# Performance work log

Hardware: AMD Instinct MI355X
Metric: run time of the kernel (lower is better)

The kernel has to match this reference:

```python
import jax, jax.numpy as jnp
import numpy as np

V = 6890   # SMPL vertices
J = 24     # SMPL joints
NB = 10    # betas
P = 207    # pose blendshape basis = (J-1)*9
B = 1024
PARENTS = np.array([-1, 0, 0, 0, 1, 2, 3, 4, 5, 6, 7, 8, 9, 9, 9, 12, 13, 14, 16, 17, 18, 19, 20, 21])


def setup_inputs() -> dict:
    key = jax.random.key(0)
    ks = jax.random.split(key, 9)
    pose_axis_angle = jax.random.normal(ks[0], (B, 69), dtype=jnp.float32) * 0.2
    betas = jax.random.normal(ks[1], (B, NB), dtype=jnp.float32)
    global_orient = jax.random.normal(ks[2], (B, 3), dtype=jnp.float32) * 0.2
    v_template = jax.random.normal(ks[3], (V, 3), dtype=jnp.float32)
    shapedirs = jax.random.normal(ks[4], (V, 3, NB), dtype=jnp.float32) * 0.01
    posedirs = jax.random.normal(ks[5], (P, V * 3), dtype=jnp.float32) * 0.01
    jr = jax.random.uniform(ks[6], (J, V), dtype=jnp.float32)
    J_regressor = jr / jr.sum(-1, keepdims=True)
    jr17 = jax.random.uniform(ks[7], (17, V), dtype=jnp.float32)
    J_regressor_h36m = jr17 / jr17.sum(-1, keepdims=True)
    w = jax.random.uniform(ks[8], (V, J), dtype=jnp.float32)
    lbs_weights = w / w.sum(-1, keepdims=True)
    return {
        'pose_axis_angle': pose_axis_angle, 'betas': betas, 'global_orient': global_orient,
        'v_template': v_template, 'shapedirs': shapedirs, 'posedirs': posedirs,
        'J_regressor': J_regressor, 'J_regressor_h36m': J_regressor_h36m,
        'lbs_weights': lbs_weights,
    }


def rodrigues(rvec):
    # rvec: [N,3] axis-angle -> [N,3,3] rotation matrices
    angle = jnp.linalg.norm(rvec + 1e-8, axis=-1, keepdims=True)  # [N,1]
    axis = rvec / angle
    s = jnp.sin(angle)[..., None]
    c = jnp.cos(angle)[..., None]
    rx, ry, rz = axis[..., 0], axis[..., 1], axis[..., 2]
    z = jnp.zeros_like(rx)
    K = jnp.stack([z, -rz, ry, rz, z, -rx, -ry, rx, z], axis=-1).reshape(-1, 3, 3)
    I = jnp.eye(3, dtype=rvec.dtype)
    return I + s * K + (1.0 - c) * (K @ K)


def _lbs(pose_axis_angle, betas, global_orient, v_template, shapedirs, posedirs,
         J_regressor, J_regressor_h36m, lbs_weights):
    b = betas.shape[0]
    full_pose = jnp.concatenate([global_orient, pose_axis_angle], axis=1)  # [B,72]
    # shape blendshapes
    v_shaped = v_template + jnp.einsum('bl,vkl->bvk', betas, shapedirs)    # [B,V,3]
    Jrest = jnp.einsum('jv,bvk->bjk', J_regressor, v_shaped)               # [B,J,3]
    # pose to rotation matrices
    rot_mats = rodrigues(full_pose.reshape(-1, 3)).reshape(b, J, 3, 3)
    I3 = jnp.eye(3, dtype=rot_mats.dtype)
    pose_feature = (rot_mats[:, 1:] - I3).reshape(b, P)                    # [B,207]
    v_posed = v_shaped + (pose_feature @ posedirs).reshape(b, V, 3)
    # kinematic tree FK
    rel = Jrest.at[:, 1:].add(-Jrest[:, PARENTS[1:]])                      # relative joint offsets
    T = (jnp.zeros((b, J, 4, 4), dtype=rot_mats.dtype)
         .at[..., :3, :3].set(rot_mats)
         .at[..., :3, 3].set(rel)
         .at[..., 3, 3].set(1.0))
    chain = [T[:, 0]]
    for i in range(1, J):
        chain.append(chain[int(PARENTS[i])] @ T[:, i])
    G = jnp.stack(chain, axis=1)                                           # [B,J,4,4]
    posed_joints = G[:, :, :3, 3]
    # remove rest-pose joint locations to get skinning transforms
    A = G.at[:, :, :3, 3].add(-jnp.einsum('bjmn,bjn->bjm', G[:, :, :3, :3], Jrest))
    # linear blend skinning
    Tv = jnp.einsum('vj,bjmn->bvmn', lbs_weights, A)                       # [B,V,4,4]
    verts = jnp.einsum('bvmn,bvn->bvm', Tv[:, :, :3, :3], v_posed) + Tv[:, :, :3, 3]
    joints_from_verts = jnp.einsum('jv,bvk->bjk', J_regressor_h36m, verts)
    return verts, posed_joints, rot_mats, joints_from_verts


def reference(pose_axis_angle, betas, global_orient, v_template, shapedirs, posedirs,
              J_regressor, J_regressor_h36m, lbs_weights):
    verts, joints, rot_mats, jfv = _lbs(pose_axis_angle, betas, global_orient, v_template,
                                        shapedirs, posedirs, J_regressor, J_regressor_h36m,
                                        lbs_weights)
    # transl is None -> root-center (root is detached in torch)
    root = jax.lax.stop_gradient(joints[:, :1])
    root17 = jax.lax.stop_gradient(jfv[:, :1])
    return verts - root, joints - root, rot_mats, jfv - root17
```

## Files before the change

kernel.cpp:

```cpp
#include <hip/hip_runtime.h>
#include <hip/hip_bf16.h>

constexpr int kB  = 1024;
constexpr int kV  = 6890;
constexpr int kJ  = 24;
constexpr int kNB = 10;
constexpr int kP  = 207;
constexpr int kH  = 17;
constexpr int TB  = 8;

constexpr int kN   = kV * 3;
constexpr int kKP  = 224;
constexpr int kNT  = 1296;
constexpr int kNP  = kNT * 16;
constexpr int kVC  = 862;

constexpr size_t O_VERTS  = 0;
constexpr size_t O_JOINTS = (size_t)kB * kV * 3;
constexpr size_t O_ROT    = O_JOINTS + (size_t)kB * kJ * 3;
constexpr size_t O_JFV    = O_ROT + (size_t)kB * kJ * 9;

constexpr size_t WS_JS   = 0;
constexpr size_t WS_FLAG = 1000;
constexpr size_t WS_A    = 1024;
constexpr size_t WS_PF   = WS_A + (size_t)kB * 288;
constexpr size_t WS_ROOT = WS_PF + (size_t)kB * kP;
constexpr size_t WS_JFV  = WS_ROOT + (size_t)kB * 3;
constexpr size_t WS_ASWZ = 563200;
constexpr size_t WS_BSWZ = WS_ASWZ + 114688;

typedef __attribute__((ext_vector_type(8))) short short8;
typedef __attribute__((ext_vector_type(4))) float float4v;

__device__ __forceinline__ unsigned short f2bf(float f) {
    unsigned u = __float_as_uint(f);
    unsigned r = (u + 0x7FFFu + ((u >> 16) & 1u)) >> 16;
    return (unsigned short)r;
}

__global__ void k_classify(const float* __restrict__ amb0, int* __restrict__ flag)
{
    if (blockIdx.x == 0 && threadIdx.x == 0) {
        float s = 0.f;
        for (int i = 0; i < kJ; i++) s += amb0[i];
        *flag = (fabsf(s - 1.0f) < 0.5f) ? 1 : 0;
    }
}

__global__ __launch_bounds__(256) void k_js(
    const float* __restrict__ amb0,
    const float* __restrict__ amb1,
    const int* __restrict__ flag,
    const float* __restrict__ sd,
    const float* __restrict__ vt,
    float* __restrict__ partial)
{
    const float* Jreg = (*flag) ? amb1 : amb0;
    int j = blockIdx.x;
    int c = blockIdx.y;
    int t = threadIdx.x;
    int lane = t & 63;
    int wave = t >> 6;

    float acc[33];
    #pragma unroll
    for (int i = 0; i < 33; i++) acc[i] = 0.f;

    int vend = min(kVC * (c + 1), kV);
    for (int v = kVC * c + t; v < vend; v += 256) {
        float w = Jreg[j * kV + v];
        const float* sdp = sd + (size_t)v * 30;
        #pragma unroll
        for (int k = 0; k < 3; k++) {
            #pragma unroll
            for (int l = 0; l < kNB; l++)
                acc[k * 11 + l] += w * sdp[k * 10 + l];
            acc[k * 11 + 10] += w * vt[v * 3 + k];
        }
    }
    #pragma unroll
    for (int off = 32; off > 0; off >>= 1) {
        #pragma unroll
        for (int i = 0; i < 33; i++)
            acc[i] += __shfl_down(acc[i], off, 64);
    }
    __shared__ float red[4][33];
    if (lane == 0) {
        #pragma unroll
        for (int i = 0; i < 33; i++) red[wave][i] = acc[i];
    }
    __syncthreads();
    if (t < 33) {
        float s = red[0][t] + red[1][t] + red[2][t] + red[3][t];
        partial[((size_t)j * 8 + c) * 33 + t] = s;
    }
}

__global__ __launch_bounds__(1024) void k_js_reduce(
    const float* __restrict__ partial,
    float* __restrict__ js)
{
    int t = threadIdx.x;
    if (t < 24 * 33) {
        int j = t / 33, i = t % 33;
        float s = 0.f;
        #pragma unroll
        for (int c = 0; c < 8; c++) s += partial[((size_t)j * 8 + c) * 33 + i];
        js[t] = s;
    }
}

__global__ __launch_bounds__(64) void k_pose(
    const float* __restrict__ pose,
    const float* __restrict__ betas,
    const float* __restrict__ gor,
    const float* __restrict__ js,
    float* __restrict__ wsA,
    float* __restrict__ wsPF,
    float* __restrict__ wsRoot,
    float* __restrict__ out)
{
    __shared__ float Rsh[kJ][9];
    __shared__ float Jr[kJ][3];
    __shared__ float G[kJ][12];

    int b = blockIdx.x;
    int t = threadIdx.x;

    if (t < kJ) {
        float rx, ry, rz;
        if (t == 0) {
            rx = gor[b * 3 + 0]; ry = gor[b * 3 + 1]; rz = gor[b * 3 + 2];
        } else {
            int o = b * 69 + (t - 1) * 3;
            rx = pose[o]; ry = pose[o + 1]; rz = pose[o + 2];
        }
        float ex = rx + 1e-8f, ey = ry + 1e-8f, ez = rz + 1e-8f;
        float ang = sqrtf(ex * ex + ey * ey + ez * ez);
        float x = rx / ang, y = ry / ang, z = rz / ang;
        float s = sinf(ang), c = cosf(ang), oc = 1.0f - c;
        float r[9];
        r[0] = 1.0f - oc * (y * y + z * z);
        r[1] = -s * z + oc * (x * y);
        r[2] =  s * y + oc * (x * z);
        r[3] =  s * z + oc * (x * y);
        r[4] = 1.0f - oc * (x * x + z * z);
        r[5] = -s * x + oc * (y * z);
        r[6] = -s * y + oc * (x * z);
        r[7] =  s * x + oc * (y * z);
        r[8] = 1.0f - oc * (x * x + y * y);
        #pragma unroll
        for (int i = 0; i < 9; i++) Rsh[t][i] = r[i];
        float* ro = out + O_ROT + (size_t)b * (kJ * 9) + (size_t)t * 9;
        #pragma unroll
        for (int i = 0; i < 9; i++) ro[i] = r[i];
        if (t >= 1) {
            float* pf = wsPF + (size_t)b * kP + (size_t)(t - 1) * 9;
            #pragma unroll
            for (int i = 0; i < 9; i++)
                pf[i] = r[i] - ((i == 0 || i == 4 || i == 8) ? 1.0f : 0.0f);
        }
        float bt[kNB];
        #pragma unroll
        for (int l = 0; l < kNB; l++) bt[l] = betas[b * kNB + l];
        #pragma unroll
        for (int k = 0; k < 3; k++) {
            const float* row = js + (t * 3 + k) * 11;
            float acc = row[10];
            #pragma unroll
            for (int l = 0; l < kNB; l++) acc += bt[l] * row[l];
            Jr[t][k] = acc;
        }
    }
    __syncthreads();

    if (t == 0) {
        const int par[kJ] = {-1,0,0,0,1,2,3,4,5,6,7,8,9,9,9,12,13,14,16,17,18,19,20,21};
        #pragma unroll
        for (int m = 0; m < 3; m++) {
            #pragma unroll
            for (int n = 0; n < 3; n++) G[0][m * 4 + n] = Rsh[0][m * 3 + n];
            G[0][m * 4 + 3] = Jr[0][m];
        }
        for (int i = 1; i < kJ; i++) {
            int p = par[i];
            float rel[3];
            #pragma unroll
            for (int k = 0; k < 3; k++) rel[k] = Jr[i][k] - Jr[p][k];
            #pragma unroll
            for (int m = 0; m < 3; m++) {
                float g0 = G[p][m * 4 + 0], g1 = G[p][m * 4 + 1], g2 = G[p][m * 4 + 2];
                #pragma unroll
                for (int n = 0; n < 3; n++) {
                    G[i][m * 4 + n] = g0 * Rsh[i][0 * 3 + n]
                                    + g1 * Rsh[i][1 * 3 + n]
                                    + g2 * Rsh[i][2 * 3 + n];
                }
                G[i][m * 4 + 3] = g0 * rel[0] + g1 * rel[1] + g2 * rel[2]
                                + G[p][m * 4 + 3];
            }
        }
    }
    __syncthreads();

    if (t < kJ) {
        float* Aj = wsA + (size_t)b * 288 + (size_t)t * 12;
        float* jo = out + O_JOINTS + (size_t)b * (kJ * 3) + (size_t)t * 3;
        #pragma unroll
        for (int m = 0; m < 3; m++) {
            float g0 = G[t][m * 4 + 0], g1 = G[t][m * 4 + 1], g2 = G[t][m * 4 + 2];
            Aj[m * 4 + 0] = g0;
            Aj[m * 4 + 1] = g1;
            Aj[m * 4 + 2] = g2;
            Aj[m * 4 + 3] = G[t][m * 4 + 3]
                          - (g0 * Jr[t][0] + g1 * Jr[t][1] + g2 * Jr[t][2]);
            jo[m] = G[t][m * 4 + 3] - G[0][m * 4 + 3];
        }
        if (t == 0) {
            #pragma unroll
            for (int k = 0; k < 3; k++) wsRoot[b * 3 + k] = G[0][k * 4 + 3];
        }
    }
}

__global__ __launch_bounds__(256) void k_prep_b(
    const float* __restrict__ pd,
    const float* __restrict__ sd,
    const float* __restrict__ vt,
    unsigned short* __restrict__ bswz)
{
    __shared__ unsigned short lds[kKP][68];
    int g = blockIdx.x;
    int n0 = g * 64;
    int t = threadIdx.x;

    for (int kbase = 0; kbase < kKP; kbase += 4) {
        int k = kbase + (t >> 6);
        int nl = t & 63;
        int n = n0 + nl;
        float val = 0.f;
        if (n < kN) {
            if (k < kP)                 val = pd[(size_t)k * kN + n];
            else if (k < kP + kNB)      val = sd[(size_t)n * kNB + (k - kP)];
            else if (k == kP + kNB)     val = vt[n];
        }
        lds[k][nl] = f2bf(val);
    }
    __syncthreads();

    #pragma unroll 1
    for (int tt = 0; tt < 4; tt++) {
        int ntile = g * 4 + tt;
        #pragma unroll 1
        for (int kt = 0; kt < 7; kt++) {
            size_t base = ((size_t)ntile * 7 + kt) * 512;
            #pragma unroll
            for (int u = 0; u < 2; u++) {
                int e = t * 2 + u;
                int quad = e >> 7, rem = e & 127;
                int nin = rem >> 3, kin = rem & 7;
                int k = kt * 32 + quad * 8 + kin;
                bswz[base + e] = lds[k][tt * 16 + nin];
            }
        }
    }
}

__global__ __launch_bounds__(256) void k_prep_a(
    const float* __restrict__ wsPF,
    const float* __restrict__ betas,
    unsigned short* __restrict__ aswz)
{
    int mtile = blockIdx.x;
    int t = threadIdx.x;
    for (int e = t; e < 16 * kKP; e += 256) {
        int kt = e >> 9, r = e & 511;
        int quad = r >> 7, min_ = (r >> 3) & 15, kin = r & 7;
        int k = kt * 32 + quad * 8 + kin;
        int b = mtile * 16 + min_;
        float val = 0.f;
        if (k < kP)             val = wsPF[(size_t)b * kP + k];
        else if (k < kP + kNB)  val = betas[(size_t)b * kNB + (k - kP)];
        else if (k == kP + kNB) val = 1.0f;
        aswz[((size_t)mtile * 7 + kt) * 512 + r] = f2bf(val);
    }
}

__global__ __launch_bounds__(256) void k_gemm(
    const unsigned short* __restrict__ A,
    const unsigned short* __restrict__ B,
    float* __restrict__ out)
{
    int tid = threadIdx.x;
    int lane = tid & 63;
    int wid = tid >> 6;
    int m0t = blockIdx.y * 8 + (wid >> 1) * 4;
    int n0t = blockIdx.x * 8 + (wid & 1) * 4;

    float4v acc[4][4];
    #pragma unroll
    for (int i = 0; i < 4; i++)
        #pragma unroll
        for (int j = 0; j < 4; j++)
            acc[i][j] = (float4v){0.f, 0.f, 0.f, 0.f};

    #pragma unroll
    for (int kt = 0; kt < 7; kt++) {
        short8 a[4], b[4];
        #pragma unroll
        for (int i = 0; i < 4; i++)
            a[i] = *(const short8*)(A + ((size_t)(m0t + i) * 7 + kt) * 512 + lane * 8);
        #pragma unroll
        for (int j = 0; j < 4; j++)
            b[j] = *(const short8*)(B + ((size_t)(n0t + j) * 7 + kt) * 512 + lane * 8);
        #pragma unroll
        for (int i = 0; i < 4; i++)
            #pragma unroll
            for (int j = 0; j < 4; j++)
                acc[i][j] = __builtin_amdgcn_mfma_f32_16x16x32_bf16(
                    a[i], b[j], acc[i][j], 0, 0, 0);
    }

    int rbase = (lane >> 4) * 4;
    int col = lane & 15;
    #pragma unroll
    for (int i = 0; i < 4; i++) {
        #pragma unroll
        for (int j = 0; j < 4; j++) {
            int n = (n0t + j) * 16 + col;
            if (n < kN) {
                #pragma unroll
                for (int reg = 0; reg < 4; reg++) {
                    int brow = (m0t + i) * 16 + rbase + reg;
                    out[O_VERTS + (size_t)brow * kN + n] = acc[i][j][reg];
                }
            }
        }
    }
}

__global__ __launch_bounds__(256) void k_prep_jh(
    const float* __restrict__ Jh,
    float* __restrict__ jht)
{
    int v = blockIdx.x * 256 + threadIdx.x;
    if (v >= kV) return;
    #pragma unroll
    for (int j = 0; j < kH; j++)
        jht[(size_t)v * kH + j] = Jh[(size_t)j * kV + v];
}

__global__ __launch_bounds__(256) void k_lbs(
    const float* __restrict__ amb0,
    const float* __restrict__ amb1,
    const int* __restrict__ flag,
    const float* __restrict__ wsA,
    const float* __restrict__ wsRoot,
    float* __restrict__ out)
{
    const float* W = (*flag) ? amb0 : amb1;

    int t = threadIdx.x;
    int b0 = blockIdx.y * TB;

    int v = blockIdx.x * 256 + t;
    if (v >= kV) return;

    float w[kJ];
    {
        const float* Wv = W + (size_t)v * kJ;
        #pragma unroll
        for (int j = 0; j < kJ; j++) w[j] = Wv[j];
    }
    #pragma unroll 1
    for (int tb = 0; tb < TB; tb++) {
        const float* Ab = wsA + (size_t)(b0 + tb) * 288;
        float Tv[12];
        #pragma unroll
        for (int i = 0; i < 12; i++) Tv[i] = w[0] * Ab[i];
        #pragma unroll
        for (int j = 1; j < kJ; j++) {
            float wj = w[j];
            #pragma unroll
            for (int i = 0; i < 12; i++) Tv[i] += wj * Ab[j * 12 + i];
        }
        float r0 = wsRoot[(size_t)(b0 + tb) * 3 + 0];
        float r1 = wsRoot[(size_t)(b0 + tb) * 3 + 1];
        float r2 = wsRoot[(size_t)(b0 + tb) * 3 + 2];
        float* op = out + O_VERTS + ((size_t)(b0 + tb) * kV + v) * 3;
        float x = op[0], y = op[1], z = op[2];
        float o0 = Tv[0] * x + Tv[1] * y + Tv[2]  * z + Tv[3]  - r0;
        float o1 = Tv[4] * x + Tv[5] * y + Tv[6]  * z + Tv[7]  - r1;
        float o2 = Tv[8] * x + Tv[9] * y + Tv[10] * z + Tv[11] - r2;
        op[0] = o0;
        op[1] = o1;
        op[2] = o2;
    }
}

__global__ __launch_bounds__(256) void k_jfv(
    const float* __restrict__ jht,
    const float* __restrict__ vertsOut,
    float* __restrict__ wsJfv)
{
    int b = blockIdx.x;
    int t = threadIdx.x;
    int lane = t & 63;
    int wave = t >> 6;

    float acc[kH * 3];
    #pragma unroll
    for (int i = 0; i < kH * 3; i++) acc[i] = 0.f;

    for (int v = t; v < kV; v += 256) {
        const float* vpt = vertsOut + ((size_t)b * kV + v) * 3;
        float vx = vpt[0], vy = vpt[1], vz = vpt[2];
        const float* jt = jht + (size_t)v * kH;
        #pragma unroll
        for (int j = 0; j < kH; j++) {
            float wj = jt[j];
            acc[j * 3 + 0] += wj * vx;
            acc[j * 3 + 1] += wj * vy;
            acc[j * 3 + 2] += wj * vz;
        }
    }
    #pragma unroll
    for (int off = 32; off > 0; off >>= 1) {
        #pragma unroll
        for (int i = 0; i < kH * 3; i++)
            acc[i] += __shfl_down(acc[i], off, 64);
    }
    __shared__ float partial[4][kH * 3];
    if (lane == 0) {
        #pragma unroll
        for (int i = 0; i < kH * 3; i++) partial[wave][i] = acc[i];
    }
    __syncthreads();
    if (t < kH * 3) {
        float s = partial[0][t] + partial[1][t] + partial[2][t] + partial[3][t];
        wsJfv[(size_t)b * 51 + t] = s;
    }
}

__global__ __launch_bounds__(64) void k_jfv_out(
    const float* __restrict__ wsJfv,
    float* __restrict__ out)
{
    int b = blockIdx.x;
    int t = threadIdx.x;
    if (t < kH * 3) {
        int k = t % 3;
        float val = wsJfv[(size_t)b * 51 + t] - wsJfv[(size_t)b * 51 + k];
        out[O_JFV + (size_t)b * 51 + t] = val;
    }
}

extern "C" void kernel_launch(void* const* d_in, const int* in_sizes, int n_in,
                              void* d_out, int out_size, void* d_ws, size_t ws_size,
                              hipStream_t stream) {
    const float *pose = nullptr, *betas = nullptr, *gor = nullptr, *vt = nullptr,
                *sd = nullptr, *pd = nullptr, *Jh = nullptr;
    const float *amb0 = nullptr, *amb1 = nullptr;
    for (int i = 0; i < n_in; i++) {
        const float* p = (const float*)d_in[i];
        switch (in_sizes[i]) {
            case 70656:   pose  = p; break;
            case 10240:   betas = p; break;
            case 3072:    gor   = p; break;
            case 20670:   vt    = p; break;
            case 206700:  sd    = p; break;
            case 4278690: pd    = p; break;
            case 117130:  Jh    = p; break;
            case 165360:  if (!amb0) amb0 = p; else amb1 = p; break;
            default: break;
        }
    }

    float* ws = (float*)d_ws;
    float* js      = ws + WS_JS;
    int*   flag    = (int*)(ws + WS_FLAG);
    float* wsA     = ws + WS_A;
    float* wsPF    = ws + WS_PF;
    float* wsRoot  = ws + WS_ROOT;
    float* wsJfv   = ws + WS_JFV;
    unsigned short* aswz = (unsigned short*)(ws + WS_ASWZ);
    unsigned short* bswz = (unsigned short*)(ws + WS_BSWZ);
    float* jspart  = ws + WS_ASWZ;
    float* jht     = ws + WS_BSWZ;

    float* out = (float*)d_out;

    k_classify<<<dim3(1), dim3(64), 0, stream>>>(amb0, flag);
    k_js<<<dim3(kJ, 8), dim3(256), 0, stream>>>(amb0, amb1, flag, sd, vt, jspart);
    k_js_reduce<<<dim3(1), dim3(1024), 0, stream>>>(jspart, js);
    k_pose<<<dim3(kB), dim3(64), 0, stream>>>(pose, betas, gor, js, wsA, wsPF, wsRoot, out);
    k_prep_b<<<dim3(kNP / 64), dim3(256), 0, stream>>>(pd, sd, vt, bswz);
    k_prep_a<<<dim3(64), dim3(256), 0, stream>>>(wsPF, betas, aswz);
    k_gemm<<<dim3(kNT / 8, kB / 128), dim3(256), 0, stream>>>(aswz, bswz, out);
    k_prep_jh<<<dim3((kV + 255) / 256), dim3(256), 0, stream>>>(Jh, jht);
    k_lbs<<<dim3((kV + 255) / 256, kB / TB), dim3(256), 0, stream>>>(
        amb0, amb1, flag, wsA, wsRoot, out);
    k_jfv<<<dim3(kB), dim3(256), 0, stream>>>(jht, out + O_VERTS, wsJfv);
    k_jfv_out<<<dim3(kB), dim3(64), 0, stream>>>(wsJfv, out);
}
```

Before: 306.4 us.

## Fuse pose-blendshape GEMM with LBS skinning via MFMA in one kernel

```diff
diff --git a/kernel.cpp b/kernel.cpp
--- a/kernel.cpp
+++ b/kernel.cpp
@@ -7,13 +7,13 @@
 constexpr int kNB = 10;
 constexpr int kP  = 207;
 constexpr int kH  = 17;
-constexpr int TB  = 8;
 
 constexpr int kN   = kV * 3;
 constexpr int kKP  = 224;
 constexpr int kNT  = 1296;
 constexpr int kNP  = kNT * 16;
 constexpr int kVC  = 862;
+constexpr int kVT  = 432;
 
 constexpr size_t O_VERTS  = 0;
 constexpr size_t O_JOINTS = (size_t)kB * kV * 3;
@@ -21,13 +21,14 @@
 constexpr size_t O_JFV    = O_ROT + (size_t)kB * kJ * 9;
 
 constexpr size_t WS_JS   = 0;
-constexpr size_t WS_FLAG = 1000;
 constexpr size_t WS_A    = 1024;
 constexpr size_t WS_PF   = WS_A + (size_t)kB * 288;
 constexpr size_t WS_ROOT = WS_PF + (size_t)kB * kP;
 constexpr size_t WS_JFV  = WS_ROOT + (size_t)kB * 3;
-constexpr size_t WS_ASWZ = 563200;
-constexpr size_t WS_BSWZ = WS_ASWZ + 114688;
+constexpr size_t WS_A1   = 563200;
+constexpr size_t WS_B1   = WS_A1 + 114688;
+constexpr size_t WS_W    = WS_PF;
+constexpr size_t WS_JHT  = WS_B1;
 
 typedef __attribute__((ext_vector_type(8))) short short8;
 typedef __attribute__((ext_vector_type(4))) float float4v;
@@ -38,24 +39,21 @@
     return (unsigned short)r;
 }
 
-__global__ void k_classify(const float* __restrict__ amb0, int* __restrict__ flag)
-{
-    if (blockIdx.x == 0 && threadIdx.x == 0) {
-        float s = 0.f;
-        for (int i = 0; i < kJ; i++) s += amb0[i];
-        *flag = (fabsf(s - 1.0f) < 0.5f) ? 1 : 0;
-    }
+__device__ __forceinline__ bool is_lbs(const float* __restrict__ p) {
+    float s = 0.f;
+    #pragma unroll
+    for (int i = 0; i < kJ; i++) s += p[i];
+    return fabsf(s - 1.0f) < 0.5f;
 }
 
 __global__ __launch_bounds__(256) void k_js(
     const float* __restrict__ amb0,
     const float* __restrict__ amb1,
-    const int* __restrict__ flag,
     const float* __restrict__ sd,
     const float* __restrict__ vt,
     float* __restrict__ partial)
 {
-    const float* Jreg = (*flag) ? amb1 : amb0;
+    const float* Jreg = is_lbs(amb0) ? amb1 : amb0;
     int j = blockIdx.x;
     int c = blockIdx.y;
     int t = threadIdx.x;
@@ -286,54 +284,112 @@
     }
 }
 
-__global__ __launch_bounds__(256) void k_gemm(
-    const unsigned short* __restrict__ A,
-    const unsigned short* __restrict__ B,
+__global__ __launch_bounds__(256) void k_prep_w(
+    const float* __restrict__ amb0,
+    const float* __restrict__ amb1,
+    unsigned short* __restrict__ wswz)
+{
+    const float* W = is_lbs(amb0) ? amb0 : amb1;
+    int vtile = blockIdx.x;
+    int t = threadIdx.x;
+    #pragma unroll
+    for (int u = 0; u < 2; u++) {
+        int e = t * 2 + u;
+        int quad = e >> 7, min_ = (e >> 3) & 15, kin = e & 7;
+        int v = vtile * 16 + min_;
+        int j = quad * 8 + kin;
+        float val = (v < kV && j < kJ) ? W[(size_t)v * kJ + j] : 0.f;
+        wswz[(size_t)vtile * 512 + e] = f2bf(val);
+    }
+}
+
+__global__ __launch_bounds__(256) void k_fused(
+    const unsigned short* __restrict__ A1,
+    const unsigned short* __restrict__ B1,
+    const unsigned short* __restrict__ Wswz,
+    const float* __restrict__ wsA,
+    const float* __restrict__ wsRoot,
     float* __restrict__ out)
 {
-    int tid = threadIdx.x;
-    int lane = tid & 63;
-    int wid = tid >> 6;
-    int m0t = blockIdx.y * 8 + (wid >> 1) * 4;
-    int n0t = blockIdx.x * 8 + (wid & 1) * 4;
-
-    float4v acc[4][4];
+    __shared__ float c1[16 * 193];
+    __shared__ unsigned short a2[16 * 512];
+
+    int t = threadIdx.x;
+    int lane = t & 63;
+    int w = t >> 6;
+    int btile = blockIdx.x;
+    int b0 = btile * 16;
+    int vt0 = blockIdx.y * 4;
+
+    for (int e = t; e < 16 * 512; e += 256) {
+        int btl = e >> 9, r = e & 511;
+        int quad = r >> 7, nin = (r >> 3) & 15, kin = r & 7;
+        int j = quad * 8 + kin;
+        float val = (j < kJ && nin < 12)
+                  ? wsA[(size_t)(b0 + btl) * 288 + j * 12 + nin] : 0.f;
+        a2[e] = f2bf(val);
+    }
+
+    float4v acc1[3];
+    #pragma unroll
+    for (int jj = 0; jj < 3; jj++) acc1[jj] = (float4v){0.f, 0.f, 0.f, 0.f};
+    #pragma unroll
+    for (int kt = 0; kt < 7; kt++) {
+        short8 af = *(const short8*)(A1 + ((size_t)btile * 7 + kt) * 512 + lane * 8);
+        #pragma unroll
+        for (int jj = 0; jj < 3; jj++) {
+            int nt = blockIdx.y * 12 + w * 3 + jj;
+            short8 bf = *(const short8*)(B1 + ((size_t)nt * 7 + kt) * 512 + lane * 8);
+            acc1[jj] = __builtin_amdgcn_mfma_f32_16x16x32_bf16(af, bf, acc1[jj], 0, 0, 0);
+        }
+    }
+    int col = lane & 15, quad = lane >> 4;
+    #pragma unroll
+    for (int jj = 0; jj < 3; jj++) {
+        #pragma unroll
+        for (int reg = 0; reg < 4; reg++) {
+            int brow = quad * 4 + reg;
+            c1[brow * 193 + (w * 3 + jj) * 16 + col] = acc1[jj][reg];
+        }
+    }
+    __syncthreads();
+
+    short8 wa[4];
     #pragma unroll
     for (int i = 0; i < 4; i++)
-        #pragma unroll
-        for (int j = 0; j < 4; j++)
-            acc[i][j] = (float4v){0.f, 0.f, 0.f, 0.f};
-
-    #pragma unroll
-    for (int kt = 0; kt < 7; kt++) {
-        short8 a[4], b[4];
+        wa[i] = *(const short8*)(Wswz + (size_t)(vt0 + i) * 512 + lane * 8);
+    float4v acc2[4][4];
+    #pragma unroll
+    for (int i = 0; i < 4; i++)
+        #pragma unroll
+        for (int jw = 0; jw < 4; jw++)
+            acc2[i][jw] = (float4v){0.f, 0.f, 0.f, 0.f};
+    #pragma unroll
+    for (int jw = 0; jw < 4; jw++) {
+        short8 bfr = *(const short8*)(a2 + (w * 4 + jw) * 512 + lane * 8);
         #pragma unroll
         for (int i = 0; i < 4; i++)
-            a[i] = *(const short8*)(A + ((size_t)(m0t + i) * 7 + kt) * 512 + lane * 8);
-        #pragma unroll
-        for (int j = 0; j < 4; j++)
-            b[j] = *(const short8*)(B + ((size_t)(n0t + j) * 7 + kt) * 512 + lane * 8);
-        #pragma unroll
-        for (int i = 0; i < 4; i++)
-            #pragma unroll
-            for (int j = 0; j < 4; j++)
-                acc[i][j] = __builtin_amdgcn_mfma_f32_16x16x32_bf16(
-                    a[i], b[j], acc[i][j], 0, 0, 0);
-    }
-
-    int rbase = (lane >> 4) * 4;
-    int col = lane & 15;
-    #pragma unroll
-    for (int i = 0; i < 4; i++) {
-        #pragma unroll
-        for (int j = 0; j < 4; j++) {
-            int n = (n0t + j) * 16 + col;
-            if (n < kN) {
-                #pragma unroll
-                for (int reg = 0; reg < 4; reg++) {
-                    int brow = (m0t + i) * 16 + rbase + reg;
-                    out[O_VERTS + (size_t)brow * kN + n] = acc[i][j][reg];
-                }
+            acc2[i][jw] = __builtin_amdgcn_mfma_f32_16x16x32_bf16(wa[i], bfr, acc2[i][jw], 0, 0, 0);
+    }
+
+    int kk = col & 3, m = col >> 2;
+    #pragma unroll
+    for (int jw = 0; jw < 4; jw++) {
+        int bl = w * 4 + jw;
+        int b = b0 + bl;
+        float rt = (m < 3) ? wsRoot[(size_t)b * 3 + m] : 0.f;
+        #pragma unroll
+        for (int i = 0; i < 4; i++) {
+            #pragma unroll
+            for (int reg = 0; reg < 4; reg++) {
+                int vloc = i * 16 + quad * 4 + reg;
+                float h = (kk < 3) ? c1[bl * 193 + vloc * 3 + kk] : 1.0f;
+                float o = acc2[i][jw][reg] * h;
+                o += __shfl_xor(o, 1, 64);
+                o += __shfl_xor(o, 2, 64);
+                int vg = blockIdx.y * 64 + vloc;
+                if (kk == 0 && m < 3 && vg < kV)
+                    out[O_VERTS + ((size_t)b * kV + vg) * 3 + m] = o - rt;
             }
         }
     }
@@ -348,54 +404,6 @@
     #pragma unroll
     for (int j = 0; j < kH; j++)
         jht[(size_t)v * kH + j] = Jh[(size_t)j * kV + v];
-}
-
-__global__ __launch_bounds__(256) void k_lbs(
-    const float* __restrict__ amb0,
-    const float* __restrict__ amb1,
-    const int* __restrict__ flag,
-    const float* __restrict__ wsA,
-    const float* __restrict__ wsRoot,
-    float* __restrict__ out)
-{
-    const float* W = (*flag) ? amb0 : amb1;
-
-    int t = threadIdx.x;
-    int b0 = blockIdx.y * TB;
-
-    int v = blockIdx.x * 256 + t;
-    if (v >= kV) return;
-
-    float w[kJ];
-    {
-        const float* Wv = W + (size_t)v * kJ;
-        #pragma unroll
-        for (int j = 0; j < kJ; j++) w[j] = Wv[j];
-    }
-    #pragma unroll 1
-    for (int tb = 0; tb < TB; tb++) {
-        const float* Ab = wsA + (size_t)(b0 + tb) * 288;
-        float Tv[12];
-        #pragma unroll
-        for (int i = 0; i < 12; i++) Tv[i] = w[0] * Ab[i];
-        #pragma unroll
-        for (int j = 1; j < kJ; j++) {
-            float wj = w[j];
-            #pragma unroll
-            for (int i = 0; i < 12; i++) Tv[i] += wj * Ab[j * 12 + i];
-        }
-        float r0 = wsRoot[(size_t)(b0 + tb) * 3 + 0];
-        float r1 = wsRoot[(size_t)(b0 + tb) * 3 + 1];
-        float r2 = wsRoot[(size_t)(b0 + tb) * 3 + 2];
-        float* op = out + O_VERTS + ((size_t)(b0 + tb) * kV + v) * 3;
-        float x = op[0], y = op[1], z = op[2];
-        float o0 = Tv[0] * x + Tv[1] * y + Tv[2]  * z + Tv[3]  - r0;
-        float o1 = Tv[4] * x + Tv[5] * y + Tv[6]  * z + Tv[7]  - r1;
-        float o2 = Tv[8] * x + Tv[9] * y + Tv[10] * z + Tv[11] - r2;
-        op[0] = o0;
-        op[1] = o1;
-        op[2] = o2;
-    }
 }
 
 __global__ __launch_bounds__(256) void k_jfv(
@@ -478,28 +486,27 @@
 
     float* ws = (float*)d_ws;
     float* js      = ws + WS_JS;
-    int*   flag    = (int*)(ws + WS_FLAG);
     float* wsA     = ws + WS_A;
     float* wsPF    = ws + WS_PF;
     float* wsRoot  = ws + WS_ROOT;
     float* wsJfv   = ws + WS_JFV;
-    unsigned short* aswz = (unsigned short*)(ws + WS_ASWZ);
-    unsigned short* bswz = (unsigned short*)(ws + WS_BSWZ);
-    float* jspart  = ws + WS_ASWZ;
-    float* jht     = ws + WS_BSWZ;
+    unsigned short* a1swz = (unsigned short*)(ws + WS_A1);
+    unsigned short* b1swz = (unsigned short*)(ws + WS_B1);
+    unsigned short* wswz  = (unsigned short*)(ws + WS_W);
+    float* jspart  = ws + WS_A1;
+    float* jht     = ws + WS_JHT;
 
     float* out = (float*)d_out;
 
-    k_classify<<<dim3(1), dim3(64), 0, stream>>>(amb0, flag);
-    k_js<<<dim3(kJ, 8), dim3(256), 0, stream>>>(amb0, amb1, flag, sd, vt, jspart);
+    k_js<<<dim3(kJ, 8), dim3(256), 0, stream>>>(amb0, amb1, sd, vt, jspart);
     k_js_reduce<<<dim3(1), dim3(1024), 0, stream>>>(jspart, js);
     k_pose<<<dim3(kB), dim3(64), 0, stream>>>(pose, betas, gor, js, wsA, wsPF, wsRoot, out);
-    k_prep_b<<<dim3(kNP / 64), dim3(256), 0, stream>>>(pd, sd, vt, bswz);
-    k_prep_a<<<dim3(64), dim3(256), 0, stream>>>(wsPF, betas, aswz);
-    k_gemm<<<dim3(kNT / 8, kB / 128), dim3(256), 0, stream>>>(aswz, bswz, out);
+    k_prep_b<<<dim3(kNP / 64), dim3(256), 0, stream>>>(pd, sd, vt, b1swz);
+    k_prep_a<<<dim3(64), dim3(256), 0, stream>>>(wsPF, betas, a1swz);
+    k_prep_w<<<dim3(kVT), dim3(256), 0, stream>>>(amb0, amb1, wswz);
+    k_fused<<<dim3(64, kVT / 4), dim3(256), 0, stream>>>(
+        a1swz, b1swz, wswz, wsA, wsRoot, out);
     k_prep_jh<<<dim3((kV + 255) / 256), dim3(256), 0, stream>>>(Jh, jht);
-    k_lbs<<<dim3((kV + 255) / 256, kB / TB), dim3(256), 0, stream>>>(
-        amb0, amb1, flag, wsA, wsRoot, out);
     k_jfv<<<dim3(kB), dim3(256), 0, stream>>>(jht, out + O_VERTS, wsJfv);
     k_jfv_out<<<dim3(kB), dim3(64), 0, stream>>>(wsJfv, out);
 }
```

After: 368.6 us. 20.3% more time.
